# Kernel optimization log

Hardware: AMD Instinct MI355X
Metric: run time of the kernel (lower is better)

## Reference

```python
import jax, jax.numpy as jnp
import numpy as np

H = 192
W = 192
EPS = 1e-6


def _quat_to_rotmat(q):
    q = q / jnp.linalg.norm(q, axis=-1, keepdims=True)
    w, x, y, z = q[..., 0], q[..., 1], q[..., 2], q[..., 3]
    R = jnp.stack([
        1 - 2 * (y * y + z * z), 2 * (x * y - w * z), 2 * (x * z + w * y),
        2 * (x * y + w * z), 1 - 2 * (x * x + z * z), 2 * (y * z - w * x),
        2 * (x * z - w * y), 2 * (y * z + w * x), 1 - 2 * (x * x + y * y)],
        axis=-1)
    return R.reshape(q.shape[:-1] + (3, 3))


def _render(means, quats, scales, opacities, colors, betas, viewmats, Ks):
    B = viewmats.shape[0]
    N = means.shape[0]
    Rw = viewmats[:, :3, :3]                                  # [B,3,3]
    tw = viewmats[:, :3, 3]                                   # [B,3]
    # world -> camera
    p = jnp.einsum('bij,nj->bni', Rw, means) + tw[:, None, :]  # [B,N,3]
    # 3D covariance from quat + exp(scale): Sigma = M M^T, M = R_q diag(s)
    Rq = _quat_to_rotmat(quats)                                # [N,3,3]
    M = Rq * jnp.exp(scales)[:, None, :]
    cov3d = jnp.einsum('nij,nkj->nik', M, M)                   # [N,3,3]
    covc = jnp.einsum('bij,njk,blk->bnil', Rw, cov3d, Rw)      # [B,N,3,3]
    tx, ty = p[..., 0], p[..., 1]
    tz = jnp.maximum(p[..., 2], 1e-2)
    fx = Ks[:, 0, 0][:, None]
    fy = Ks[:, 1, 1][:, None]
    cx = Ks[:, 0, 2][:, None]
    cy = Ks[:, 1, 2][:, None]
    z1 = 1.0 / tz
    zero = jnp.zeros_like(tz)
    # perspective Jacobian [B,N,2,3]
    J = jnp.stack([
        jnp.stack([fx * z1, zero, -fx * tx * z1 * z1], axis=-1),
        jnp.stack([zero, fy * z1, -fy * ty * z1 * z1], axis=-1)], axis=-2)
    cov2d = jnp.einsum('bnij,bnjk,bnlk->bnil', J, covc, J)     # [B,N,2,2]
    a = cov2d[..., 0, 0] + 0.3                                 # screen-space blur (gsplat)
    b = cov2d[..., 0, 1]
    c = cov2d[..., 1, 1] + 0.3
    det = a * c - b * b
    u = fx * tx * z1 + cx
    v = fy * ty * z1 + cy
    # global front-to-back depth sort (non-packed reference)
    order = jnp.argsort(p[..., 2], axis=-1)                    # [B,N]

    def g(x):
        return jnp.take_along_axis(x, order, axis=1)

    u, v, a, b, c, det = g(u), g(v), g(a), g(b), g(c), g(det)
    tz_s = g(tz)
    op = g(jnp.broadcast_to(jax.nn.sigmoid(opacities)[None], (B, N)))
    bt = g(jnp.broadcast_to(betas[None], (B, N)))
    col = jnp.take_along_axis(
        jnp.broadcast_to(colors[None], (B, N, 3)),
        jnp.broadcast_to(order[..., None], (B, N, 3)), axis=1)
    inv_det = 1.0 / jnp.maximum(det, EPS)
    Ac = c * inv_det
    Bc = -b * inv_det
    Cc = a * inv_det
    xs = jnp.arange(W, dtype=jnp.float32) + 0.5
    ys = jnp.arange(H, dtype=jnp.float32) + 0.5
    dx = xs[None, None, :, None] - u[:, None, None, :]         # [B,H,W,N]
    dy = ys[None, :, None, None] - v[:, None, None, :]         # [B,H,W,N]
    sigma = 0.5 * (Ac[:, None, None, :] * dx * dx
                   + Cc[:, None, None, :] * dy * dy) \
            + Bc[:, None, None, :] * dx * dy
    sigma = jnp.maximum(sigma, 1e-8)
    # generalized-gaussian kernel with per-splat beta exponent
    alpha = op[:, None, None, :] * jnp.exp(-sigma ** bt[:, None, None, :])
    valid = (p[..., 2] > 1e-2)
    valid = jnp.take_along_axis(valid, order, axis=1) & (det > EPS)
    alpha = jnp.where(valid[:, None, None, :], alpha, 0.0)
    alpha = jnp.minimum(alpha, 0.999)
    alpha = jnp.where(alpha > 1.0 / 255.0, alpha, 0.0)
    T = jnp.cumprod(1.0 - alpha, axis=-1)
    T_excl = jnp.concatenate([jnp.ones_like(T[..., :1]), T[..., :-1]], axis=-1)
    w = alpha * T_excl                                         # [B,H,W,N]
    rgb = jnp.einsum('bhwn,bnc->bhwc', w, col)                 # [B,H,W,3]
    acc = jnp.sum(w, axis=-1)                                  # [B,H,W]
    return rgb, acc


def setup_inputs() -> dict:
    key = jax.random.key(0)
    ks = jax.random.split(key, 8)
    N = 512
    xy = (jax.random.uniform(ks[0], (N, 2)) - 0.5) * 4.0
    z = jax.random.uniform(ks[1], (N, 1)) * 6.0 + 2.0
    means = jnp.concatenate([xy, z], axis=1)
    quats = jax.random.normal(ks[2], (N, 4))
    scales = jax.random.normal(ks[3], (N, 3)) * 0.3 + np.log(0.05).astype(np.float32)
    opacities = jax.random.normal(ks[4], (N,))
    colors = jax.random.uniform(ks[5], (N, 3))
    betas = jnp.ones((N,), dtype=jnp.float32)
    viewmats = jnp.eye(4, dtype=jnp.float32)[None]
    Ks = jnp.array([[[220.0, 0.0, 96.0], [0.0, 220.0, 96.0], [0.0, 0.0, 1.0]]],
                   dtype=jnp.float32)
    return {'means': means, 'quats': quats, 'scales': scales,
            'opacities': opacities, 'colors': colors, 'betas': betas,
            'viewmats': viewmats, 'Ks': Ks}


def reference(means, quats, scales, opacities, colors, betas, viewmats, Ks):
    rgb, acc = _render(means, quats, scales, opacities, colors, betas,
                       viewmats, Ks)
    return rgb, acc
```

## Files before the change

kernel.cpp:

```cpp
#include <hip/hip_runtime.h>
#include <hip/hip_bf16.h>

#define NG 512
#define IMG_H 192
#define IMG_W 192
#define NPIX (IMG_H * IMG_W)
#define GF 10
#define NCHUNK 8

__global__ __launch_bounds__(NG) void preprocess_kernel(
    const float* __restrict__ means, const float* __restrict__ quats,
    const float* __restrict__ scales, const float* __restrict__ opac,
    const float* __restrict__ colors, const float* __restrict__ betas,
    const float* __restrict__ vm, const float* __restrict__ Ks,
    float* __restrict__ ws)
{
    __shared__ float zsh[NG];
    const int g = threadIdx.x;

    const float Rw[3][3] = {{vm[0], vm[1], vm[2]},
                            {vm[4], vm[5], vm[6]},
                            {vm[8], vm[9], vm[10]}};
    const float tw[3] = {vm[3], vm[7], vm[11]};
    const float fx = Ks[0], cx = Ks[2], fy = Ks[4], cy = Ks[5];

    const float mx = means[g*3+0], my = means[g*3+1], mz = means[g*3+2];
    const float px = Rw[0][0]*mx + Rw[0][1]*my + Rw[0][2]*mz + tw[0];
    const float py = Rw[1][0]*mx + Rw[1][1]*my + Rw[1][2]*mz + tw[1];
    const float pz = Rw[2][0]*mx + Rw[2][1]*my + Rw[2][2]*mz + tw[2];
    zsh[g] = pz;

    float qw = quats[g*4+0], qx = quats[g*4+1], qy = quats[g*4+2], qz = quats[g*4+3];
    const float qn = 1.0f / sqrtf(qw*qw + qx*qx + qy*qy + qz*qz);
    qw *= qn; qx *= qn; qy *= qn; qz *= qn;
    float Rq[3][3];
    Rq[0][0] = 1.f - 2.f*(qy*qy + qz*qz); Rq[0][1] = 2.f*(qx*qy - qw*qz); Rq[0][2] = 2.f*(qx*qz + qw*qy);
    Rq[1][0] = 2.f*(qx*qy + qw*qz); Rq[1][1] = 1.f - 2.f*(qx*qx + qz*qz); Rq[1][2] = 2.f*(qy*qz - qw*qx);
    Rq[2][0] = 2.f*(qx*qz - qw*qy); Rq[2][1] = 2.f*(qy*qz + qw*qx); Rq[2][2] = 1.f - 2.f*(qx*qx + qy*qy);

    const float e0 = expf(scales[g*3+0]);
    const float e1 = expf(scales[g*3+1]);
    const float e2 = expf(scales[g*3+2]);

    float M[3][3];
    #pragma unroll
    for (int i = 0; i < 3; i++) { M[i][0] = Rq[i][0]*e0; M[i][1] = Rq[i][1]*e1; M[i][2] = Rq[i][2]*e2; }
    float c3[3][3];
    #pragma unroll
    for (int i = 0; i < 3; i++)
        #pragma unroll
        for (int k = 0; k < 3; k++)
            c3[i][k] = M[i][0]*M[k][0] + M[i][1]*M[k][1] + M[i][2]*M[k][2];

    float tmp[3][3];
    #pragma unroll
    for (int i = 0; i < 3; i++)
        #pragma unroll
        for (int k = 0; k < 3; k++)
            tmp[i][k] = Rw[i][0]*c3[0][k] + Rw[i][1]*c3[1][k] + Rw[i][2]*c3[2][k];
    float S[3][3];
    #pragma unroll
    for (int i = 0; i < 3; i++)
        #pragma unroll
        for (int l = 0; l < 3; l++)
            S[i][l] = tmp[i][0]*Rw[l][0] + tmp[i][1]*Rw[l][1] + tmp[i][2]*Rw[l][2];

    const float tz = fmaxf(pz, 0.01f);
    const float z1 = 1.0f / tz;
    const float j0 = fx*z1, j2 = -fx*px*z1*z1;
    const float j1 = fy*z1, j3 = -fy*py*z1*z1;

    const float cov00 = j0*j0*S[0][0] + 2.f*j0*j2*S[0][2] + j2*j2*S[2][2];
    const float cov01 = j0*j1*S[0][1] + j0*j3*S[0][2] + j2*j1*S[1][2] + j2*j3*S[2][2];
    const float cov11 = j1*j1*S[1][1] + 2.f*j1*j3*S[1][2] + j3*j3*S[2][2];

    const float a = cov00 + 0.3f;
    const float b = cov01;
    const float c = cov11 + 0.3f;
    const float det = a*c - b*b;
    const float u = fx*px*z1 + cx;
    const float v = fy*py*z1 + cy;
    const bool valid = (pz > 0.01f) && (det > 1e-6f);
    const float inv_det = 1.0f / fmaxf(det, 1e-6f);
    const float Ac = c * inv_det;
    const float Bc = -b * inv_det;
    const float Cc = a * inv_det;
    float op = 1.0f / (1.0f + expf(-opac[g]));
    if (!valid) op = 0.0f;

    __syncthreads();
    int rank = 0;
    #pragma unroll 8
    for (int j = 0; j < NG; j++) {
        const float zj = zsh[j];
        rank += (zj < pz) || (zj == pz && j < g);
    }

    float* dst = ws + rank * GF;
    dst[0] = u;  dst[1] = v;  dst[2] = Ac; dst[3] = Bc; dst[4] = Cc;
    dst[5] = op; dst[6] = betas[g];
    dst[7] = colors[g*3+0]; dst[8] = colors[g*3+1]; dst[9] = colors[g*3+2];
}

__global__ __launch_bounds__(512) void render_kernel(
    const float* __restrict__ ws, float* __restrict__ out)
{
    __shared__ __align__(16) float gs[NG * GF];
    __shared__ int clist[NG];
    __shared__ float part[NCHUNK * 64 * 5];
    __shared__ int wcnt[NCHUNK];
    __shared__ int woff[NCHUNK + 1];

    const int tid  = threadIdx.x;
    const int lane = tid & 63;
    const int wv   = tid >> 6;

    {
        const float4* src = (const float4*)ws;
        float4* dst = (float4*)gs;
        for (int i = tid; i < NG * GF / 4; i += 512) dst[i] = src[i];
    }
    __syncthreads();

    const int strip = blockIdx.x;
    const int y  = strip / 3;
    const int x0 = (strip % 3) * 64;
    const float fyp = (float)y + 0.5f;
    const float xlo = (float)x0 + 0.5f;
    const float xhi = (float)x0 + 63.5f;

    {
        const float* gp = gs + tid * GF;
        const float u = gp[0], v = gp[1], A = gp[2], B = gp[3], C = gp[4];
        const float op = gp[5], bt = gp[6];
        const float dy = fyp - v;
        const float dxlo = xlo - u, dxhi = xhi - u;
        float dxs = -B * dy / fmaxf(A, 1e-12f);
        dxs = fminf(fmaxf(dxs, dxlo), dxhi);
        float smin = 0.5f * (A * dxs * dxs + C * dy * dy) + B * dxs * dy;
        smin = fmaxf(smin, 1e-8f);
        const float se = (bt == 1.0f) ? smin : powf(smin, bt);
        const float amax = op * expf(-se);
        const bool keep = amax > (1.0f / 255.0f);

        const unsigned long long m = __ballot(keep);
        if (lane == 0) wcnt[wv] = __popcll(m);
        __syncthreads();
        if (tid == 0) {
            int s = 0;
            #pragma unroll
            for (int k = 0; k < NCHUNK; k++) { woff[k] = s; s += wcnt[k]; }
            woff[NCHUNK] = s;
        }
        __syncthreads();
        if (keep) {
            const int pos = woff[wv] + __popcll(m & ((1ULL << lane) - 1));
            clist[pos] = tid;
        }
    }
    __syncthreads();

    const int total = woff[NCHUNK];
    const int s = (wv * total) >> 3;
    const int e = ((wv + 1) * total) >> 3;

    const float fxp = (float)(x0 + lane) + 0.5f;
    float T = 1.0f, cr = 0.0f, cg = 0.0f, cb = 0.0f, ac = 0.0f;
    for (int i = s; i < e; i++) {
        const float* gp = gs + clist[i] * GF;
        const float dx = fxp - gp[0];
        const float dy = fyp - gp[1];
        float sigma = 0.5f * (gp[2]*dx*dx + gp[4]*dy*dy) + gp[3]*dx*dy;
        sigma = fmaxf(sigma, 1e-8f);
        const float bt = gp[6];
        const float se = (bt == 1.0f) ? sigma : powf(sigma, bt);
        float alpha = gp[5] * expf(-se);
        alpha = fminf(alpha, 0.999f);
        if (!(alpha > (1.0f / 255.0f))) alpha = 0.0f;
        const float w = alpha * T;
        cr += w * gp[7]; cg += w * gp[8]; cb += w * gp[9];
        ac += w;
        T *= 1.0f - alpha;
    }

    float* pp = part + (wv * 64 + lane) * 5;
    pp[0] = cr; pp[1] = cg; pp[2] = cb; pp[3] = ac; pp[4] = T;
    __syncthreads();

    if (wv == 0) {
        float Tt = 1.0f, r = 0.0f, g = 0.0f, b = 0.0f, a = 0.0f;
        #pragma unroll
        for (int k = 0; k < NCHUNK; k++) {
            const float* pk = part + (k * 64 + lane) * 5;
            r += Tt * pk[0]; g += Tt * pk[1]; b += Tt * pk[2]; a += Tt * pk[3];
            Tt *= pk[4];
        }
        const int pix = y * IMG_W + x0 + lane;
        out[pix * 3 + 0] = r;
        out[pix * 3 + 1] = g;
        out[pix * 3 + 2] = b;
        out[NPIX * 3 + pix] = a;
    }
}

extern "C" void kernel_launch(void* const* d_in, const int* in_sizes, int n_in,
                              void* d_out, int out_size, void* d_ws, size_t ws_size,
                              hipStream_t stream) {
    const float* means  = (const float*)d_in[0];
    const float* quats  = (const float*)d_in[1];
    const float* scales = (const float*)d_in[2];
    const float* opac   = (const float*)d_in[3];
    const float* colors = (const float*)d_in[4];
    const float* betas  = (const float*)d_in[5];
    const float* vm     = (const float*)d_in[6];
    const float* Ks     = (const float*)d_in[7];
    float* ws  = (float*)d_ws;
    float* out = (float*)d_out;

    preprocess_kernel<<<1, NG, 0, stream>>>(means, quats, scales, opac, colors, betas, vm, Ks, ws);
    render_kernel<<<NPIX / 64, 512, 0, stream>>>(ws, out);
}
```

Measured before the change: 85.49 us.

## Fuse preprocessing into render kernel, recomputing projection and sort per block

Merges the single-block preprocess kernel into the render kernel. Every one of the 576 blocks now projects all 512 gaussians and ranks them by depth itself, writing the sorted records straight into shared memory. This removes a kernel launch, the serial dependency on a one-block kernel, and the global workspace round trip. In exchange each block repeats the O(N^2) rank loop and the per-gaussian math, which adds redundant compute to every block.

```diff
diff --git a/kernel.cpp b/kernel.cpp
--- a/kernel.cpp
+++ b/kernel.cpp
@@ -8,15 +8,23 @@
 #define GF 10
 #define NCHUNK 8
 
-__global__ __launch_bounds__(NG) void preprocess_kernel(
+__global__ __launch_bounds__(512) void splat_kernel(
     const float* __restrict__ means, const float* __restrict__ quats,
     const float* __restrict__ scales, const float* __restrict__ opac,
     const float* __restrict__ colors, const float* __restrict__ betas,
     const float* __restrict__ vm, const float* __restrict__ Ks,
-    float* __restrict__ ws)
+    float* __restrict__ out)
 {
     __shared__ float zsh[NG];
-    const int g = threadIdx.x;
+    __shared__ __align__(16) float gs[NG * GF];
+    __shared__ int clist[NG];
+    __shared__ float part[NCHUNK * 64 * 5];
+    __shared__ int wcnt[NCHUNK];
+    __shared__ int woff[NCHUNK + 1];
+
+    const int tid  = threadIdx.x;
+    const int lane = tid & 63;
+    const int wv   = tid >> 6;
 
     const float Rw[3][3] = {{vm[0], vm[1], vm[2]},
                             {vm[4], vm[5], vm[6]},
@@ -24,6 +32,7 @@
     const float tw[3] = {vm[3], vm[7], vm[11]};
     const float fx = Ks[0], cx = Ks[2], fy = Ks[4], cy = Ks[5];
 
+    const int g = tid;
     const float mx = means[g*3+0], my = means[g*3+1], mz = means[g*3+2];
     const float px = Rw[0][0]*mx + Rw[0][1]*my + Rw[0][2]*mz + tw[0];
     const float py = Rw[1][0]*mx + Rw[1][1]*my + Rw[1][2]*mz + tw[1];
@@ -52,18 +61,18 @@
         for (int k = 0; k < 3; k++)
             c3[i][k] = M[i][0]*M[k][0] + M[i][1]*M[k][1] + M[i][2]*M[k][2];
 
-    float tmp[3][3];
+    float tmpm[3][3];
     #pragma unroll
     for (int i = 0; i < 3; i++)
         #pragma unroll
         for (int k = 0; k < 3; k++)
-            tmp[i][k] = Rw[i][0]*c3[0][k] + Rw[i][1]*c3[1][k] + Rw[i][2]*c3[2][k];
+            tmpm[i][k] = Rw[i][0]*c3[0][k] + Rw[i][1]*c3[1][k] + Rw[i][2]*c3[2][k];
     float S[3][3];
     #pragma unroll
     for (int i = 0; i < 3; i++)
         #pragma unroll
         for (int l = 0; l < 3; l++)
-            S[i][l] = tmp[i][0]*Rw[l][0] + tmp[i][1]*Rw[l][1] + tmp[i][2]*Rw[l][2];
+            S[i][l] = tmpm[i][0]*Rw[l][0] + tmpm[i][1]*Rw[l][1] + tmpm[i][2]*Rw[l][2];
 
     const float tz = fmaxf(pz, 0.01f);
     const float z1 = 1.0f / tz;
@@ -82,9 +91,6 @@
     const float v = fy*py*z1 + cy;
     const bool valid = (pz > 0.01f) && (det > 1e-6f);
     const float inv_det = 1.0f / fmaxf(det, 1e-6f);
-    const float Ac = c * inv_det;
-    const float Bc = -b * inv_det;
-    const float Cc = a * inv_det;
     float op = 1.0f / (1.0f + expf(-opac[g]));
     if (!valid) op = 0.0f;
 
@@ -95,30 +101,14 @@
         const float zj = zsh[j];
         rank += (zj < pz) || (zj == pz && j < g);
     }
-
-    float* dst = ws + rank * GF;
-    dst[0] = u;  dst[1] = v;  dst[2] = Ac; dst[3] = Bc; dst[4] = Cc;
-    dst[5] = op; dst[6] = betas[g];
-    dst[7] = colors[g*3+0]; dst[8] = colors[g*3+1]; dst[9] = colors[g*3+2];
-}
-
-__global__ __launch_bounds__(512) void render_kernel(
-    const float* __restrict__ ws, float* __restrict__ out)
-{
-    __shared__ __align__(16) float gs[NG * GF];
-    __shared__ int clist[NG];
-    __shared__ float part[NCHUNK * 64 * 5];
-    __shared__ int wcnt[NCHUNK];
-    __shared__ int woff[NCHUNK + 1];
-
-    const int tid  = threadIdx.x;
-    const int lane = tid & 63;
-    const int wv   = tid >> 6;
-
     {
-        const float4* src = (const float4*)ws;
-        float4* dst = (float4*)gs;
-        for (int i = tid; i < NG * GF / 4; i += 512) dst[i] = src[i];
+        float* dst = gs + rank * GF;
+        dst[0] = u;  dst[1] = v;
+        dst[2] = c * inv_det;
+        dst[3] = -b * inv_det;
+        dst[4] = a * inv_det;
+        dst[5] = op; dst[6] = betas[g];
+        dst[7] = colors[g*3+0]; dst[8] = colors[g*3+1]; dst[9] = colors[g*3+2];
     }
     __syncthreads();
 
@@ -131,16 +121,16 @@
 
     {
         const float* gp = gs + tid * GF;
-        const float u = gp[0], v = gp[1], A = gp[2], B = gp[3], C = gp[4];
-        const float op = gp[5], bt = gp[6];
-        const float dy = fyp - v;
-        const float dxlo = xlo - u, dxhi = xhi - u;
+        const float gu = gp[0], gv = gp[1], A = gp[2], B = gp[3], C = gp[4];
+        const float gop = gp[5], bt = gp[6];
+        const float dy = fyp - gv;
+        const float dxlo = xlo - gu, dxhi = xhi - gu;
         float dxs = -B * dy / fmaxf(A, 1e-12f);
         dxs = fminf(fmaxf(dxs, dxlo), dxhi);
         float smin = 0.5f * (A * dxs * dxs + C * dy * dy) + B * dxs * dy;
         smin = fmaxf(smin, 1e-8f);
         const float se = (bt == 1.0f) ? smin : powf(smin, bt);
-        const float amax = op * expf(-se);
+        const float amax = gop * expf(-se);
         const bool keep = amax > (1.0f / 255.0f);
 
         const unsigned long long m = __ballot(keep);
@@ -188,18 +178,18 @@
     __syncthreads();
 
     if (wv == 0) {
-        float Tt = 1.0f, r = 0.0f, g = 0.0f, b = 0.0f, a = 0.0f;
+        float Tt = 1.0f, r = 0.0f, gg = 0.0f, bb = 0.0f, aa = 0.0f;
         #pragma unroll
         for (int k = 0; k < NCHUNK; k++) {
             const float* pk = part + (k * 64 + lane) * 5;
-            r += Tt * pk[0]; g += Tt * pk[1]; b += Tt * pk[2]; a += Tt * pk[3];
+            r += Tt * pk[0]; gg += Tt * pk[1]; bb += Tt * pk[2]; aa += Tt * pk[3];
             Tt *= pk[4];
         }
         const int pix = y * IMG_W + x0 + lane;
         out[pix * 3 + 0] = r;
-        out[pix * 3 + 1] = g;
-        out[pix * 3 + 2] = b;
-        out[NPIX * 3 + pix] = a;
+        out[pix * 3 + 1] = gg;
+        out[pix * 3 + 2] = bb;
+        out[NPIX * 3 + pix] = aa;
     }
 }
 
@@ -214,9 +204,8 @@
     const float* betas  = (const float*)d_in[5];
     const float* vm     = (const float*)d_in[6];
     const float* Ks     = (const float*)d_in[7];
-    float* ws  = (float*)d_ws;
     float* out = (float*)d_out;
 
-    preprocess_kernel<<<1, NG, 0, stream>>>(means, quats, scales, opac, colors, betas, vm, Ks, ws);
-    render_kernel<<<NPIX / 64, 512, 0, stream>>>(ws, out);
+    splat_kernel<<<NPIX / 64, 512, 0, stream>>>(
+        means, quats, scales, opac, colors, betas, vm, Ks, out);
 }
```

After: 98.92 us. +15.7%, slower.

## Split depth-rank computation across 4 blocks and 4 segments per Gaussian

Applied to the files above, without the earlier changes.

The preprocess kernel now runs 4 blocks of 512 threads. Each block recomputes all depths into shared memory, then 4 thread segments count partial ranks over 128 depths each using float4 loads. The partial counts are summed, and only the first segment finishes the per-Gaussian preprocessing. The record stride is padded from 10 to 12 floats so the render kernel's shared-memory copy becomes a fixed, fully unrolled loop. This shortens the serial 512-iteration rank loop on a single block, at the cost of redundant depth computation and extra synchronisation.

```diff
diff --git a/kernel.cpp b/kernel.cpp
--- a/kernel.cpp
+++ b/kernel.cpp
@@ -5,18 +5,24 @@
 #define IMG_H 192
 #define IMG_W 192
 #define NPIX (IMG_H * IMG_W)
-#define GF 10
+#define GF 12
 #define NCHUNK 8
 
-__global__ __launch_bounds__(NG) void preprocess_kernel(
+__global__ __launch_bounds__(512) void preprocess_kernel(
     const float* __restrict__ means, const float* __restrict__ quats,
     const float* __restrict__ scales, const float* __restrict__ opac,
     const float* __restrict__ colors, const float* __restrict__ betas,
     const float* __restrict__ vm, const float* __restrict__ Ks,
     float* __restrict__ ws)
 {
-    __shared__ float zsh[NG];
-    const int g = threadIdx.x;
+    __shared__ __align__(16) float zsh[NG];
+    __shared__ int rpart[4 * 128];
+
+    const int tid = threadIdx.x;
+    const int blk = blockIdx.x;
+    const int gl  = tid & 127;
+    const int seg = tid >> 7;
+    const int g   = blk * 128 + gl;
 
     const float Rw[3][3] = {{vm[0], vm[1], vm[2]},
                             {vm[4], vm[5], vm[6]},
@@ -24,11 +30,38 @@
     const float tw[3] = {vm[3], vm[7], vm[11]};
     const float fx = Ks[0], cx = Ks[2], fy = Ks[4], cy = Ks[5];
 
+    {
+        const float ax = means[tid*3+0], ay = means[tid*3+1], az = means[tid*3+2];
+        zsh[tid] = Rw[2][0]*ax + Rw[2][1]*ay + Rw[2][2]*az + tw[2];
+    }
+    __syncthreads();
+
+    const float zg = zsh[g];
+    int cnt = 0;
+    {
+        const float4* z4 = (const float4*)(zsh + seg * 128);
+        const int jbase = seg * 128;
+        #pragma unroll 8
+        for (int i = 0; i < 32; i++) {
+            const float4 zz = z4[i];
+            const int j = jbase + 4 * i;
+            cnt += (zz.x < zg) || (zz.x == zg && (j + 0) < g);
+            cnt += (zz.y < zg) || (zz.y == zg && (j + 1) < g);
+            cnt += (zz.z < zg) || (zz.z == zg && (j + 2) < g);
+            cnt += (zz.w < zg) || (zz.w == zg && (j + 3) < g);
+        }
+    }
+    rpart[seg * 128 + gl] = cnt;
+    __syncthreads();
+
+    if (seg != 0) return;
+
+    const int rank = rpart[gl] + rpart[128 + gl] + rpart[256 + gl] + rpart[384 + gl];
+
     const float mx = means[g*3+0], my = means[g*3+1], mz = means[g*3+2];
     const float px = Rw[0][0]*mx + Rw[0][1]*my + Rw[0][2]*mz + tw[0];
     const float py = Rw[1][0]*mx + Rw[1][1]*my + Rw[1][2]*mz + tw[1];
-    const float pz = Rw[2][0]*mx + Rw[2][1]*my + Rw[2][2]*mz + tw[2];
-    zsh[g] = pz;
+    const float pz = zg;
 
     float qw = quats[g*4+0], qx = quats[g*4+1], qy = quats[g*4+2], qz = quats[g*4+3];
     const float qn = 1.0f / sqrtf(qw*qw + qx*qx + qy*qy + qz*qz);
@@ -52,18 +85,18 @@
         for (int k = 0; k < 3; k++)
             c3[i][k] = M[i][0]*M[k][0] + M[i][1]*M[k][1] + M[i][2]*M[k][2];
 
-    float tmp[3][3];
+    float tmpm[3][3];
     #pragma unroll
     for (int i = 0; i < 3; i++)
         #pragma unroll
         for (int k = 0; k < 3; k++)
-            tmp[i][k] = Rw[i][0]*c3[0][k] + Rw[i][1]*c3[1][k] + Rw[i][2]*c3[2][k];
+            tmpm[i][k] = Rw[i][0]*c3[0][k] + Rw[i][1]*c3[1][k] + Rw[i][2]*c3[2][k];
     float S[3][3];
     #pragma unroll
     for (int i = 0; i < 3; i++)
         #pragma unroll
         for (int l = 0; l < 3; l++)
-            S[i][l] = tmp[i][0]*Rw[l][0] + tmp[i][1]*Rw[l][1] + tmp[i][2]*Rw[l][2];
+            S[i][l] = tmpm[i][0]*Rw[l][0] + tmpm[i][1]*Rw[l][1] + tmpm[i][2]*Rw[l][2];
 
     const float tz = fmaxf(pz, 0.01f);
     const float z1 = 1.0f / tz;
@@ -82,24 +115,17 @@
     const float v = fy*py*z1 + cy;
     const bool valid = (pz > 0.01f) && (det > 1e-6f);
     const float inv_det = 1.0f / fmaxf(det, 1e-6f);
-    const float Ac = c * inv_det;
-    const float Bc = -b * inv_det;
-    const float Cc = a * inv_det;
     float op = 1.0f / (1.0f + expf(-opac[g]));
     if (!valid) op = 0.0f;
 
-    __syncthreads();
-    int rank = 0;
-    #pragma unroll 8
-    for (int j = 0; j < NG; j++) {
-        const float zj = zsh[j];
-        rank += (zj < pz) || (zj == pz && j < g);
-    }
-
     float* dst = ws + rank * GF;
-    dst[0] = u;  dst[1] = v;  dst[2] = Ac; dst[3] = Bc; dst[4] = Cc;
-    dst[5] = op; dst[6] = betas[g];
-    dst[7] = colors[g*3+0]; dst[8] = colors[g*3+1]; dst[9] = colors[g*3+2];
+    dst[0]  = u;  dst[1] = v;
+    dst[2]  = c * inv_det;
+    dst[3]  = -b * inv_det;
+    dst[4]  = a * inv_det;
+    dst[5]  = op; dst[6] = betas[g];
+    dst[7]  = colors[g*3+0]; dst[8] = colors[g*3+1]; dst[9] = colors[g*3+2];
+    dst[10] = 0.0f; dst[11] = 0.0f;
 }
 
 __global__ __launch_bounds__(512) void render_kernel(
@@ -118,7 +144,9 @@
     {
         const float4* src = (const float4*)ws;
         float4* dst = (float4*)gs;
-        for (int i = tid; i < NG * GF / 4; i += 512) dst[i] = src[i];
+        #pragma unroll
+        for (int i = 0; i < NG * GF / 4 / 512; i++)
+            dst[tid + i * 512] = src[tid + i * 512];
     }
     __syncthreads();
 
@@ -217,6 +245,6 @@
     float* ws  = (float*)d_ws;
     float* out = (float*)d_out;
 
-    preprocess_kernel<<<1, NG, 0, stream>>>(means, quats, scales, opac, colors, betas, vm, Ks, ws);
+    preprocess_kernel<<<4, 512, 0, stream>>>(means, quats, scales, opac, colors, betas, vm, Ks, ws);
     render_kernel<<<NPIX / 64, 512, 0, stream>>>(ws, out);
 }
```

Result: faster. 75.44 us (-11.8%).
